# Performance work log

Measured on AMD Instinct MI355X. Metric: run time of the kernel, lower is better.

The kernel has to match this reference:

```python
import jax, jax.numpy as jnp
import numpy as np

MASK_ID = -100
L, D, HID, NH = 10, 768, 3072, 12
DH = D // NH
REACH = 2  # (sliding_window_size - 1) // 2 with window 5


def _layernorm(x, g, b, eps=1e-5):
    mu = x.mean(-1, keepdims=True)
    var = ((x - mu) ** 2).mean(-1, keepdims=True)
    return (x - mu) * jax.lax.rsqrt(var + eps) * g + b


def _adaln(x, temb, w, bb, g, be):
    # AdaLayerNormShiftScale: linear(silu(temb)) -> (scale, shift)
    e = jax.nn.silu(temb) @ w + bb
    scale, shift = jnp.split(e, 2, axis=-1)
    return _layernorm(x, g, be) * (1.0 + scale) + shift


def _timestep_emb(t):
    half = D // 2
    exponent = -np.log(10000.0) * jnp.arange(half, dtype=jnp.float32) / (half - 1.0)
    freq = jnp.exp(exponent)  # [half]
    emb = t.astype(jnp.float32)[..., None] * freq  # [b,s,half]
    return jnp.concatenate([jnp.sin(emb), jnp.cos(emb)], axis=-1)  # [b,s,D]


def setup_inputs():
    key = jax.random.key(0)
    ks = jax.random.split(key, 16)
    b, s = 4, 1024
    # packed token ids: 4 samples of 256 tokens (16x16 grid), last 64 tokens padding
    idx = np.arange(s)
    sid = idx // 256
    hpos = (idx % 256) // 16
    wpos = idx % 16
    sid = np.where(idx >= 960, MASK_ID, sid)
    tok = np.stack([sid, hpos, wpos], axis=-1)  # [s,3]
    token_ids = jnp.asarray(np.broadcast_to(tok, (b, s, 3)).copy(), dtype=jnp.int32)
    t = jax.random.randint(ks[0], (b, 1), 0, L + 1).astype(jnp.int32)
    t = jnp.broadcast_to(t, (b, s))

    def w(k, shape):
        return jax.random.normal(k, shape, jnp.float32) * 0.02

    return dict(
        x=jax.random.normal(ks[1], (b, s, D), jnp.float32),
        t=t,
        token_ids=token_ids,
        proj_in_w=w(ks[2], (D, D)), proj_in_b=jnp.zeros((D,), jnp.float32),
        h_emb=w(ks[3], (64, D)), w_emb=w(ks[4], (64, D)),
        adaln1_w=w(ks[5], (L, D, 2 * D)), adaln1_b=jnp.zeros((L, 2 * D), jnp.float32),
        ln1_g=jnp.ones((L, D), jnp.float32), ln1_b=jnp.zeros((L, D), jnp.float32),
        qkv_w=w(ks[6], (L, D, 3 * D)), qkv_b=jnp.zeros((L, 3 * D), jnp.float32),
        o_w=w(ks[7], (L, D, D)), o_b=jnp.zeros((L, D), jnp.float32),
        adaln2_w=w(ks[8], (L, D, 2 * D)), adaln2_b=jnp.zeros((L, 2 * D), jnp.float32),
        ln2_g=jnp.ones((L, D), jnp.float32), ln2_b=jnp.zeros((L, D), jnp.float32),
        fc1_w=w(ks[9], (L, D, HID)), fc1_b=jnp.zeros((L, HID), jnp.float32),
        fc2_w=w(ks[10], (L, HID, D)), fc2_b=jnp.zeros((L, D), jnp.float32),
        nout_w=w(ks[11], (D, 2 * D)), nout_b=jnp.zeros((2 * D,), jnp.float32),
        nout_g=jnp.ones((D,), jnp.float32), nout_beta=jnp.zeros((D,), jnp.float32),
    )


def _encoder(x, t, token_ids, proj_in_w, proj_in_b, h_emb, w_emb,
             adaln1_w, adaln1_b, ln1_g, ln1_b, qkv_w, qkv_b, o_w, o_b,
             adaln2_w, adaln2_b, ln2_g, ln2_b, fc1_w, fc1_b, fc2_w, fc2_b,
             nout_w, nout_b, nout_g, nout_beta):
    b, s, _ = x.shape
    sample_ids = token_ids[..., 0]          # [b,s]
    pos = token_ids[..., 1:]                # [b,s,2]
    x = x @ proj_in_w + proj_in_b
    x = x + h_emb[pos[..., 0]] + w_emb[pos[..., 1]]

    # block-sparse mask: same packed sample, Chebyshev sliding window, no padding queries
    same = sample_ids[:, :, None] == sample_ids[:, None, :]              # [b,s,s]
    cheby = jnp.abs(pos[:, :, None, :] - pos[:, None, :, :]).max(-1)      # [b,s,s]
    notpad_q = (sample_ids != MASK_ID)[:, :, None]
    mask = same & (cheby <= REACH) & notpad_q                             # [b,s,s]
    row_valid = mask.any(-1)[..., None]                                   # [b,s,1]

    temb = _timestep_emb(t)  # [b,s,D]
    scale = 1.0 / np.sqrt(DH)
    for i in range(L):
        h1 = _adaln(x, temb, adaln1_w[i], adaln1_b[i], ln1_g[i], ln1_b[i])
        qkv = h1 @ qkv_w[i] + qkv_b[i]
        q, k, v = jnp.split(qkv, 3, axis=-1)
        q = q.reshape(b, s, NH, DH)
        k = k.reshape(b, s, NH, DH)
        v = v.reshape(b, s, NH, DH)
        scores = jnp.einsum('bqhd,bkhd->bhqk', q, k) * scale
        scores = jnp.where(mask[:, None], scores, -1e30)
        attn = jax.nn.softmax(scores, axis=-1)
        o = jnp.einsum('bhqk,bkhd->bqhd', attn, v).reshape(b, s, D)
        o = jnp.where(row_valid, o, 0.0)  # fully-masked (padding) rows -> 0
        x = x + o @ o_w[i] + o_b[i]
        h2 = _adaln(x, temb, adaln2_w[i], adaln2_b[i], ln2_g[i], ln2_b[i])
        x = x + jax.nn.gelu(h2 @ fc1_w[i] + fc1_b[i], approximate=False) @ fc2_w[i] + fc2_b[i]
    x = _adaln(x, temb, nout_w, nout_b, nout_g, nout_beta)
    return x


def reference(x, t, token_ids, proj_in_w, proj_in_b, h_emb, w_emb,
              adaln1_w, adaln1_b, ln1_g, ln1_b, qkv_w, qkv_b, o_w, o_b,
              adaln2_w, adaln2_b, ln2_g, ln2_b, fc1_w, fc1_b, fc2_w, fc2_b,
              nout_w, nout_b, nout_g, nout_beta):
    return _encoder(x, t, token_ids, proj_in_w, proj_in_b, h_emb, w_emb,
                    adaln1_w, adaln1_b, ln1_g, ln1_b, qkv_w, qkv_b, o_w, o_b,
                    adaln2_w, adaln2_b, ln2_g, ln2_b, fc1_w, fc1_b, fc2_w, fc2_b,
                    nout_w, nout_b, nout_g, nout_beta)
```

## Files before the change

kernel.cpp:

```cpp
#include <hip/hip_runtime.h>
#include <hip/hip_bf16.h>
#include <math.h>

#define MASK_ID (-100)
#define SEQ 1024
#define BATCH 4
#define DMODEL 768
#define NHEAD 12
#define DHEAD 64
#define NLAYER 10
#define HIDDEN 3072

typedef unsigned short ushort_t;
typedef unsigned int uint_t;

__device__ __forceinline__ ushort_t f2bf(float f) {
    uint_t u = __float_as_uint(f);
    u = u + 0x7fffu + ((u >> 16) & 1u);
    return (ushort_t)(u >> 16);
}
__device__ __forceinline__ float bf2f(ushort_t u) {
    return __uint_as_float(((uint_t)u) << 16);
}

__device__ __forceinline__ void async_ld16(ushort_t* lds, const ushort_t* g) {
    __builtin_amdgcn_global_load_lds((__attribute__((address_space(1))) const void*)g,
                                     (__attribute__((address_space(3))) void*)lds, 16, 0, 0);
}

#define WAITVM(n) asm volatile("s_waitcnt vmcnt(" #n ")" ::: "memory")

__global__ void temb_silu_kernel(const int* __restrict__ t, float* __restrict__ stemb) {
    int b = blockIdx.x;
    int j = threadIdx.x;
    float tv = (float)t[b * SEQ];
    float freq = expf(-logf(10000.f) * (float)j / 383.f);
    float arg = tv * freq;
    float s = sinf(arg), c = cosf(arg);
    stemb[b * DMODEL + j]       = s / (1.f + expf(-s));
    stemb[b * DMODEL + 384 + j] = c / (1.f + expf(-c));
}

__global__ __launch_bounds__(256)
void adaln_partial_kernel(const float* __restrict__ stemb,
                          const float* __restrict__ a1w,
                          const float* __restrict__ a2w,
                          const float* __restrict__ nw,
                          float* __restrict__ partial) {
    int chunk = blockIdx.x;
    int kc    = blockIdx.y;
    int slot  = blockIdx.z;
    int tid = threadIdx.x;
    int col = chunk * 256 + tid;
    const float* W;
    if (slot == 20) W = nw;
    else {
        int i = slot >> 1;
        W = ((slot & 1) ? a2w : a1w) + (size_t)i * DMODEL * 2 * DMODEL;
    }
    __shared__ float sb[4 * 96];
    for (int idx = tid; idx < 4 * 96; idx += 256) {
        int bb = idx / 96, kk = idx % 96;
        sb[idx] = stemb[bb * DMODEL + kc * 96 + kk];
    }
    __syncthreads();
    const float* Wp = W + (size_t)(kc * 96) * (2 * DMODEL) + col;
    float a0 = 0.f, a1 = 0.f, a2 = 0.f, a3 = 0.f;
    #pragma unroll 4
    for (int kk = 0; kk < 96; ++kk) {
        float w = Wp[(size_t)kk * (2 * DMODEL)];
        a0 = fmaf(sb[kk], w, a0);
        a1 = fmaf(sb[96 + kk], w, a1);
        a2 = fmaf(sb[192 + kk], w, a2);
        a3 = fmaf(sb[288 + kk], w, a3);
    }
    size_t base = ((size_t)(slot * 8 + kc) * 4) * (2 * DMODEL) + col;
    partial[base + 0 * 2 * DMODEL] = a0;
    partial[base + 1 * 2 * DMODEL] = a1;
    partial[base + 2 * 2 * DMODEL] = a2;
    partial[base + 3 * 2 * DMODEL] = a3;
}

__global__ __launch_bounds__(256)
void adaln_reduce_kernel(const float* __restrict__ partial,
                         const float* __restrict__ a1b, const float* __restrict__ a2b,
                         const float* __restrict__ nb,
                         float* __restrict__ e_all) {
    int chunk = blockIdx.x;
    int slot  = blockIdx.y;
    int col = chunk * 256 + threadIdx.x;
    const float* bb;
    if (slot == 20) bb = nb;
    else {
        int i = slot >> 1;
        bb = ((slot & 1) ? a2b : a1b) + i * 2 * DMODEL;
    }
    float bias = bb[col];
    float s0 = bias, s1 = bias, s2 = bias, s3 = bias;
    #pragma unroll
    for (int kc = 0; kc < 8; ++kc) {
        size_t base = ((size_t)(slot * 8 + kc) * 4) * (2 * DMODEL) + col;
        s0 += partial[base + 0 * 2 * DMODEL];
        s1 += partial[base + 1 * 2 * DMODEL];
        s2 += partial[base + 2 * 2 * DMODEL];
        s3 += partial[base + 3 * 2 * DMODEL];
    }
    size_t o = (size_t)slot * 4 * (2 * DMODEL) + col;
    e_all[o + 0 * 2 * DMODEL] = s0;
    e_all[o + 1 * 2 * DMODEL] = s1;
    e_all[o + 2 * 2 * DMODEL] = s2;
    e_all[o + 3 * 2 * DMODEL] = s3;
}

__global__ __launch_bounds__(256)
void transpose_bf16_kernel(const float* __restrict__ in, ushort_t* __restrict__ out,
                           int R, int C) {
    __shared__ float tile[32][33];
    int tx = threadIdx.x & 31, ty = threadIdx.x >> 5;
    int c0 = blockIdx.x * 32, r0 = blockIdx.y * 32;
    #pragma unroll
    for (int i = 0; i < 4; ++i)
        tile[ty + 8 * i][tx] = in[(size_t)(r0 + ty + 8 * i) * C + c0 + tx];
    __syncthreads();
    #pragma unroll
    for (int i = 0; i < 4; ++i)
        out[(size_t)(c0 + ty + 8 * i) * R + r0 + tx] = f2bf(tile[tx][ty + 8 * i]);
}

__global__ __launch_bounds__(256)
void transpose_all_kernel(const float* __restrict__ w0, const float* __restrict__ w1,
                          const float* __restrict__ w2, const float* __restrict__ w3,
                          ushort_t* __restrict__ o0, ushort_t* __restrict__ o1,
                          ushort_t* __restrict__ o2, ushort_t* __restrict__ o3) {
    int layer = blockIdx.y;
    int id = blockIdx.x;
    const float* in; ushort_t* out; int R, C, tile_id, TX;
    if (id < 432) {
        in = w0 + (size_t)layer * DMODEL * 3 * DMODEL; out = o0 + (size_t)layer * 3 * DMODEL * DMODEL;
        R = DMODEL; C = 3 * DMODEL; tile_id = id; TX = 36;
    } else if (id < 576) {
        in = w1 + (size_t)layer * DMODEL * DMODEL; out = o1 + (size_t)layer * DMODEL * DMODEL;
        R = DMODEL; C = DMODEL; tile_id = id - 432; TX = 12;
    } else if (id < 1152) {
        in = w2 + (size_t)layer * DMODEL * HIDDEN; out = o2 + (size_t)layer * HIDDEN * DMODEL;
        R = DMODEL; C = HIDDEN; tile_id = id - 576; TX = 48;
    } else {
        in = w3 + (size_t)layer * HIDDEN * DMODEL; out = o3 + (size_t)layer * DMODEL * HIDDEN;
        R = HIDDEN; C = DMODEL; tile_id = id - 1152; TX = 12;
    }
    int c0 = (tile_id % TX) * 64, r0 = (tile_id / TX) * 64;
    __shared__ ushort_t tlb[64 * 65];
    int tid = threadIdx.x;
    #pragma unroll
    for (int i = 0; i < 16; ++i) {
        int idx = i * 256 + tid;
        int r = idx >> 6, c = idx & 63;
        tlb[r * 65 + c] = f2bf(in[(size_t)(r0 + r) * C + c0 + c]);
    }
    __syncthreads();
    #pragma unroll
    for (int j = 0; j < 8; ++j) {
        int idx = j * 256 + tid;
        int oc = idx >> 5, pr = idx & 31;
        uint_t pk = (uint_t)tlb[(pr * 2) * 65 + oc] | ((uint_t)tlb[(pr * 2 + 1) * 65 + oc] << 16);
        *(uint_t*)&out[(size_t)(c0 + oc) * R + r0 + pr * 2] = pk;
    }
}

__global__ __launch_bounds__(256)
void f32_to_bf16_kernel(const float* __restrict__ in, ushort_t* __restrict__ out, int n8) {
    int i = blockIdx.x * 256 + threadIdx.x;
    if (i >= n8) return;
    float4 a = ((const float4*)in)[2 * i];
    float4 b = ((const float4*)in)[2 * i + 1];
    uint4 o;
    o.x = (uint_t)f2bf(a.x) | ((uint_t)f2bf(a.y) << 16);
    o.y = (uint_t)f2bf(a.z) | ((uint_t)f2bf(a.w) << 16);
    o.z = (uint_t)f2bf(b.x) | ((uint_t)f2bf(b.y) << 16);
    o.w = (uint_t)f2bf(b.z) | ((uint_t)f2bf(b.w) << 16);
    ((uint4*)out)[i] = o;
}

template<int OUT_BF>
__global__ __launch_bounds__(256)
void ln_adaln_kernel(const float* __restrict__ in, void* __restrict__ outv,
                     const float* __restrict__ g, const float* __restrict__ be,
                     const float* __restrict__ e) {
    int wid = threadIdx.x >> 6, lane = threadIdx.x & 63;
    int row = blockIdx.x * 4 + wid;
    int b = row >> 10;
    const float* xr = in + (size_t)row * DMODEL;
    float v[12];
    float s = 0.f, ss = 0.f;
    #pragma unroll
    for (int j = 0; j < 12; ++j) {
        v[j] = xr[lane + j * 64];
        s += v[j];
        ss = fmaf(v[j], v[j], ss);
    }
    #pragma unroll
    for (int o = 1; o < 64; o <<= 1) { s += __shfl_xor(s, o); ss += __shfl_xor(ss, o); }
    float mu = s * (1.f / DMODEL);
    float var = ss * (1.f / DMODEL) - mu * mu;
    float rs = rsqrtf(var + 1e-5f);
    const float* esc = e + (size_t)b * (2 * DMODEL);
    #pragma unroll
    for (int j = 0; j < 12; ++j) {
        int c = lane + j * 64;
        float y = (v[j] - mu) * rs * g[c] + be[c];
        y = y * (1.f + esc[c]) + esc[DMODEL + c];
        if (OUT_BF) ((ushort_t*)outv)[(size_t)row * DMODEL + c] = f2bf(y);
        else        ((float*)outv)[(size_t)row * DMODEL + c] = y;
    }
}

__device__ __forceinline__ float gelu_exact(float x) {
    return 0.5f * x * (1.f + erff(x * 0.70710678118654752f));
}

template<int EPI>
__global__ __launch_bounds__(256, 3)
void gemm_bf16_big(const ushort_t* __restrict__ A, const ushort_t* __restrict__ Wt,
                   const float* __restrict__ bias, void* __restrict__ outv,
                   int M, int N, int K) {
    constexpr int BM = 128, BN = 128;
    using f32x4  = __attribute__((ext_vector_type(4))) float;
    using bf16x8 = __attribute__((ext_vector_type(8))) short;

    __shared__ __align__(16) ushort_t lds[(BM + BN) * 64];

    int tid = threadIdx.x;
    int lane = tid & 63, wid = tid >> 6;
    int wr = wid >> 1, wc = wid & 1;
    int l16 = lane & 15, lg = lane >> 4;
    int sw = l16 & 7;

    int nx = N / BN;
    int cpx = gridDim.x >> 3;
    int wg = blockIdx.x;
    int wgid = (wg & 7) * cpx + (wg >> 3);
    int bx = wgid % nx, by = wgid / nx;
    int bm0 = by * BM, bn0 = bx * BN;

    f32x4 acc[4][4];
    #pragma unroll
    for (int m = 0; m < 4; ++m)
        #pragma unroll
        for (int n = 0; n < 4; ++n)
            #pragma unroll
            for (int r = 0; r < 4; ++r) acc[m][n][r] = 0.f;

    const ushort_t* Abase = A + (size_t)bm0 * K;
    const ushort_t* Bbase = Wt + (size_t)bn0 * K;

    int nk = K >> 6;
    for (int kt = 0; kt < nk; ++kt) {
        #pragma unroll
        for (int s2 = 0; s2 < 4; ++s2) {
            int ca = s2 * 256 + tid;
            int rw = ca >> 3, kcs = (ca & 7) ^ (rw & 7);
            async_ld16(&lds[ca * 8], Abase + (size_t)rw * K + kt * 64 + kcs * 8);
        }
        #pragma unroll
        for (int s2 = 0; s2 < 4; ++s2) {
            int ca = s2 * 256 + tid;
            int rw = ca >> 3, kcs = (ca & 7) ^ (rw & 7);
            async_ld16(&lds[BM * 64 + ca * 8], Bbase + (size_t)rw * K + kt * 64 + kcs * 8);
        }
        WAITVM(0);
        __syncthreads();
        #pragma unroll
        for (int kk = 0; kk < 2; ++kk) {
            int csw = (kk * 4 + lg) ^ sw;
            bf16x8 af[4], bfr[4];
            #pragma unroll
            for (int m = 0; m < 4; ++m)
                af[m] = *(const bf16x8*)&lds[(wr * 64 + m * 16 + l16) * 64 + csw * 8];
            #pragma unroll
            for (int n = 0; n < 4; ++n)
                bfr[n] = *(const bf16x8*)&lds[BM * 64 + (wc * 64 + n * 16 + l16) * 64 + csw * 8];
            #pragma unroll
            for (int m = 0; m < 4; ++m)
                #pragma unroll
                for (int n = 0; n < 4; ++n)
                    acc[m][n] = __builtin_amdgcn_mfma_f32_16x16x32_bf16(af[m], bfr[n], acc[m][n], 0, 0, 0);
        }
        __syncthreads();
    }

    int r0 = bm0 + wr * 64, c0 = bn0 + wc * 64;
    #pragma unroll
    for (int m = 0; m < 4; ++m) {
        #pragma unroll
        for (int n = 0; n < 4; ++n) {
            int cc = c0 + n * 16 + l16;
            float bcol = bias[cc];
            #pragma unroll
            for (int r = 0; r < 4; ++r) {
                int row = r0 + m * 16 + lg * 4 + r;
                float v = acc[m][n][r] + bcol;
                if (EPI == 0) ((ushort_t*)outv)[(size_t)row * N + cc] = f2bf(v);
                else          ((ushort_t*)outv)[(size_t)row * N + cc] = f2bf(gelu_exact(v));
            }
        }
    }
}

template<int BM, int BN, int EPI, int OCC>
__global__ __launch_bounds__(256, OCC)
void gemm_bf16(const ushort_t* __restrict__ A, const ushort_t* __restrict__ Wt,
               const float* __restrict__ bias, void* __restrict__ outv,
               const float* __restrict__ emb_h, const float* __restrict__ emb_w,
               const int* __restrict__ tok,
               int M, int N, int K) {
    constexpr int WM = BM / 2, WN = BN / 2;
    constexpr int FM = WM / 16, FN = WN / 16;
    constexpr int BUF = (BM + BN) * 64;
    constexpr int LPT = (BM + BN) / 32;
    using f32x4  = __attribute__((ext_vector_type(4))) float;
    using bf16x8 = __attribute__((ext_vector_type(8))) short;

    __shared__ __align__(16) ushort_t lds[3 * BUF];

    int tid = threadIdx.x;
    int lane = tid & 63, wid = tid >> 6;
    int wr = wid >> 1, wc = wid & 1;
    int l16 = lane & 15, lg = lane >> 4;
    int sw = l16 & 7;

    int nx = N / BN;
    int cpx = gridDim.x >> 3;
    int wg = blockIdx.x;
    int wgid = (wg & 7) * cpx + (wg >> 3);
    int bx = wgid % nx, by = wgid / nx;
    int bm0 = by * BM, bn0 = bx * BN;

    f32x4 acc[FM][FN];
    #pragma unroll
    for (int m = 0; m < FM; ++m)
        #pragma unroll
        for (int n = 0; n < FN; ++n)
            #pragma unroll
            for (int r = 0; r < 4; ++r) acc[m][n][r] = 0.f;

    const ushort_t* Abase = A + (size_t)bm0 * K;
    const ushort_t* Bbase = Wt + (size_t)bn0 * K;

    #define STAGE(bufi, kt)                                                             \
        do {                                                                            \
            _Pragma("unroll")                                                           \
            for (int s2 = 0; s2 < BM / 32; ++s2) {                                      \
                int ca = s2 * 256 + tid;                                                \
                int rw = ca >> 3, kcs = (ca & 7) ^ (rw & 7);                            \
                async_ld16(&lds[(bufi) * BUF + ca * 8],                                 \
                           Abase + (size_t)rw * K + (kt) * 64 + kcs * 8);               \
            }                                                                           \
            _Pragma("unroll")                                                           \
            for (int s2 = 0; s2 < BN / 32; ++s2) {                                      \
                int ca = s2 * 256 + tid;                                                \
                int rw = ca >> 3, kcs = (ca & 7) ^ (rw & 7);                            \
                async_ld16(&lds[(bufi) * BUF + BM * 64 + ca * 8],                       \
                           Bbase + (size_t)rw * K + (kt) * 64 + kcs * 8);               \
            }                                                                           \
        } while (0)

    int nk = K >> 6;
    STAGE(0, 0);
    STAGE(1, 1);
    int bufi = 0;
    for (int kt = 0; kt < nk; ++kt) {
        int nxt = bufi + 2; if (nxt >= 3) nxt -= 3;
        if (kt + 2 < nk) {
            STAGE(nxt, kt + 2);
            if constexpr (LPT == 4) WAITVM(8); else WAITVM(12);
        } else if (kt + 1 < nk) {
            if constexpr (LPT == 4) WAITVM(4); else WAITVM(6);
        } else {
            WAITVM(0);
        }
        __builtin_amdgcn_s_barrier();
        __builtin_amdgcn_s_setprio(1);
        #pragma unroll
        for (int kk = 0; kk < 2; ++kk) {
            bf16x8 af[FM], bfr[FN];
            #pragma unroll
            for (int m = 0; m < FM; ++m) {
                int row = wr * WM + m * 16 + l16;
                int csw = (kk * 4 + lg) ^ sw;
                af[m] = *(const bf16x8*)&lds[bufi * BUF + row * 64 + csw * 8];
            }
            #pragma unroll
            for (int n = 0; n < FN; ++n) {
                int row = wc * WN + n * 16 + l16;
                int csw = (kk * 4 + lg) ^ sw;
                bfr[n] = *(const bf16x8*)&lds[bufi * BUF + BM * 64 + row * 64 + csw * 8];
            }
            #pragma unroll
            for (int m = 0; m < FM; ++m)
                #pragma unroll
                for (int n = 0; n < FN; ++n)
                    acc[m][n] = __builtin_amdgcn_mfma_f32_16x16x32_bf16(af[m], bfr[n], acc[m][n], 0, 0, 0);
        }
        __builtin_amdgcn_s_setprio(0);
        __builtin_amdgcn_s_barrier();
        ++bufi; if (bufi >= 3) bufi = 0;
    }
    #undef STAGE

    int r0 = bm0 + wr * WM, c0 = bn0 + wc * WN;
    #pragma unroll
    for (int m = 0; m < FM; ++m) {
        #pragma unroll
        for (int n = 0; n < FN; ++n) {
            int cc = c0 + n * 16 + l16;
            float bcol = bias[cc];
            #pragma unroll
            for (int r = 0; r < 4; ++r) {
                int row = r0 + m * 16 + lg * 4 + r;
                float v = acc[m][n][r] + bcol;
                if (EPI == 0) {
                    ((ushort_t*)outv)[(size_t)row * N + cc] = f2bf(v);
                } else if (EPI == 1) {
                    int p0 = tok[row * 3 + 1], p1 = tok[row * 3 + 2];
                    v += emb_h[p0 * DMODEL + cc] + emb_w[p1 * DMODEL + cc];
                    ((float*)outv)[(size_t)row * N + cc] = v;
                } else if (EPI == 2) {
                    float* op = (float*)outv + (size_t)row * N + cc;
                    *op = *op + v;
                } else {
                    ((ushort_t*)outv)[(size_t)row * N + cc] = f2bf(gelu_exact(v));
                }
            }
        }
    }
}

__global__ __launch_bounds__(256)
void attn_kernel(const ushort_t* __restrict__ qkv, const int* __restrict__ tok,
                 ushort_t* __restrict__ o_out) {
    int tid = threadIdx.x;
    int u = tid >> 2, part = tid & 3;
    int q = blockIdx.x * 16 + (u & 15);
    int h = blockIdx.y * 4 + (u >> 4);
    int b = blockIdx.z;
    int m = b * SEQ + q;
    ushort_t* op = o_out + (size_t)m * DMODEL + h * DHEAD + part * 16;
    int sid = tok[m * 3];
    if (sid == MASK_ID) {
        uint4 z = {0u, 0u, 0u, 0u};
        ((uint4*)op)[0] = z;
        ((uint4*)op)[1] = z;
        return;
    }
    int qh = tok[m * 3 + 1], qw = tok[m * 3 + 2];
    const ushort_t* qp = qkv + (size_t)m * (3 * DMODEL) + h * DHEAD + part * 16;
    float qv[16], ov[16];
    {
        uint4 u0 = ((const uint4*)qp)[0];
        uint4 u1 = ((const uint4*)qp)[1];
        qv[0] = bf2f(u0.x & 0xffff); qv[1] = bf2f(u0.x >> 16);
        qv[2] = bf2f(u0.y & 0xffff); qv[3] = bf2f(u0.y >> 16);
        qv[4] = bf2f(u0.z & 0xffff); qv[5] = bf2f(u0.z >> 16);
        qv[6] = bf2f(u0.w & 0xffff); qv[7] = bf2f(u0.w >> 16);
        qv[8]  = bf2f(u1.x & 0xffff); qv[9]  = bf2f(u1.x >> 16);
        qv[10] = bf2f(u1.y & 0xffff); qv[11] = bf2f(u1.y >> 16);
        qv[12] = bf2f(u1.z & 0xffff); qv[13] = bf2f(u1.z >> 16);
        qv[14] = bf2f(u1.w & 0xffff); qv[15] = bf2f(u1.w >> 16);
    }
    #pragma unroll
    for (int i = 0; i < 16; ++i) ov[i] = 0.f;
    float mx = -1e30f, den = 0.f;
    for (int dh = -2; dh <= 2; ++dh) {
        for (int dw = -2; dw <= 2; ++dw) {
            int kq = q + dh * 16 + dw;
            if (kq < 0 || kq >= SEQ) continue;
            int km = b * SEQ + kq;
            if (tok[km * 3] != sid) continue;
            int kh2 = tok[km * 3 + 1], kw2 = tok[km * 3 + 2];
            int adh = kh2 - qh; if (adh < 0) adh = -adh;
            int adw = kw2 - qw; if (adw < 0) adw = -adw;
            if (adh > 2 || adw > 2) continue;
            const ushort_t* kp = qkv + (size_t)km * (3 * DMODEL) + DMODEL + h * DHEAD + part * 16;
            float dot;
            {
                uint4 u0 = ((const uint4*)kp)[0];
                uint4 u1 = ((const uint4*)kp)[1];
                dot = qv[0] * bf2f(u0.x & 0xffff);
                dot = fmaf(qv[1], bf2f(u0.x >> 16), dot);
                dot = fmaf(qv[2], bf2f(u0.y & 0xffff), dot);
                dot = fmaf(qv[3], bf2f(u0.y >> 16), dot);
                dot = fmaf(qv[4], bf2f(u0.z & 0xffff), dot);
                dot = fmaf(qv[5], bf2f(u0.z >> 16), dot);
                dot = fmaf(qv[6], bf2f(u0.w & 0xffff), dot);
                dot = fmaf(qv[7], bf2f(u0.w >> 16), dot);
                dot = fmaf(qv[8],  bf2f(u1.x & 0xffff), dot);
                dot = fmaf(qv[9],  bf2f(u1.x >> 16), dot);
                dot = fmaf(qv[10], bf2f(u1.y & 0xffff), dot);
                dot = fmaf(qv[11], bf2f(u1.y >> 16), dot);
                dot = fmaf(qv[12], bf2f(u1.z & 0xffff), dot);
                dot = fmaf(qv[13], bf2f(u1.z >> 16), dot);
                dot = fmaf(qv[14], bf2f(u1.w & 0xffff), dot);
                dot = fmaf(qv[15], bf2f(u1.w >> 16), dot);
            }
            dot += __shfl_xor(dot, 1);
            dot += __shfl_xor(dot, 2);
            float sc = dot * 0.125f;
            float nm = fmaxf(mx, sc);
            float c1 = expf(mx - nm);
            float c2 = expf(sc - nm);
            den = den * c1 + c2;
            const ushort_t* vp = qkv + (size_t)km * (3 * DMODEL) + 2 * DMODEL + h * DHEAD + part * 16;
            {
                uint4 u0 = ((const uint4*)vp)[0];
                uint4 u1 = ((const uint4*)vp)[1];
                ov[0] = ov[0] * c1 + c2 * bf2f(u0.x & 0xffff);
                ov[1] = ov[1] * c1 + c2 * bf2f(u0.x >> 16);
                ov[2] = ov[2] * c1 + c2 * bf2f(u0.y & 0xffff);
                ov[3] = ov[3] * c1 + c2 * bf2f(u0.y >> 16);
                ov[4] = ov[4] * c1 + c2 * bf2f(u0.z & 0xffff);
                ov[5] = ov[5] * c1 + c2 * bf2f(u0.z >> 16);
                ov[6] = ov[6] * c1 + c2 * bf2f(u0.w & 0xffff);
                ov[7] = ov[7] * c1 + c2 * bf2f(u0.w >> 16);
                ov[8]  = ov[8]  * c1 + c2 * bf2f(u1.x & 0xffff);
                ov[9]  = ov[9]  * c1 + c2 * bf2f(u1.x >> 16);
                ov[10] = ov[10] * c1 + c2 * bf2f(u1.y & 0xffff);
                ov[11] = ov[11] * c1 + c2 * bf2f(u1.y >> 16);
                ov[12] = ov[12] * c1 + c2 * bf2f(u1.z & 0xffff);
                ov[13] = ov[13] * c1 + c2 * bf2f(u1.z >> 16);
                ov[14] = ov[14] * c1 + c2 * bf2f(u1.w & 0xffff);
                ov[15] = ov[15] * c1 + c2 * bf2f(u1.w >> 16);
            }
            mx = nm;
        }
    }
    float inv = 1.f / den;
    uint4 o0, o1;
    o0.x = (uint_t)f2bf(ov[0] * inv) | ((uint_t)f2bf(ov[1] * inv) << 16);
    o0.y = (uint_t)f2bf(ov[2] * inv) | ((uint_t)f2bf(ov[3] * inv) << 16);
    o0.z = (uint_t)f2bf(ov[4] * inv) | ((uint_t)f2bf(ov[5] * inv) << 16);
    o0.w = (uint_t)f2bf(ov[6] * inv) | ((uint_t)f2bf(ov[7] * inv) << 16);
    o1.x = (uint_t)f2bf(ov[8]  * inv) | ((uint_t)f2bf(ov[9]  * inv) << 16);
    o1.y = (uint_t)f2bf(ov[10] * inv) | ((uint_t)f2bf(ov[11] * inv) << 16);
    o1.z = (uint_t)f2bf(ov[12] * inv) | ((uint_t)f2bf(ov[13] * inv) << 16);
    o1.w = (uint_t)f2bf(ov[14] * inv) | ((uint_t)f2bf(ov[15] * inv) << 16);
    ((uint4*)op)[0] = o0;
    ((uint4*)op)[1] = o1;
}

extern "C" void kernel_launch(void* const* d_in, const int* in_sizes, int n_in,
                              void* d_out, int out_size, void* d_ws, size_t ws_size,
                              hipStream_t stream) {
    const float* x_in      = (const float*)d_in[0];
    const int*   t         = (const int*)d_in[1];
    const int*   tok       = (const int*)d_in[2];
    const float* proj_in_w = (const float*)d_in[3];
    const float* proj_in_b = (const float*)d_in[4];
    const float* h_emb     = (const float*)d_in[5];
    const float* w_emb     = (const float*)d_in[6];
    const float* adaln1_w  = (const float*)d_in[7];
    const float* adaln1_b  = (const float*)d_in[8];
    const float* ln1_g     = (const float*)d_in[9];
    const float* ln1_b     = (const float*)d_in[10];
    const float* qkv_w     = (const float*)d_in[11];
    const float* qkv_b     = (const float*)d_in[12];
    const float* o_w       = (const float*)d_in[13];
    const float* o_b       = (const float*)d_in[14];
    const float* adaln2_w  = (const float*)d_in[15];
    const float* adaln2_b  = (const float*)d_in[16];
    const float* ln2_g     = (const float*)d_in[17];
    const float* ln2_b     = (const float*)d_in[18];
    const float* fc1_w     = (const float*)d_in[19];
    const float* fc1_b     = (const float*)d_in[20];
    const float* fc2_w     = (const float*)d_in[21];
    const float* fc2_b     = (const float*)d_in[22];
    const float* nout_w    = (const float*)d_in[23];
    const float* nout_b    = (const float*)d_in[24];
    const float* nout_g    = (const float*)d_in[25];
    const float* nout_beta = (const float*)d_in[26];

    const int M = BATCH * SEQ;

    float* stemb   = (float*)d_ws;
    float* e_all   = stemb + BATCH * DMODEL;
    float* partial = e_all + 21 * BATCH * 2 * DMODEL;
    ushort_t* h_bf   = (ushort_t*)(partial + 21 * 8 * 4 * 2 * DMODEL);
    ushort_t* qkv_bf = h_bf + (size_t)M * DMODEL;
    ushort_t* hid_bf = qkv_bf + (size_t)M * 3 * DMODEL;
    ushort_t* projT  = hid_bf + (size_t)M * HIDDEN;
    ushort_t* qkvT_a = projT + (size_t)DMODEL * DMODEL;
    ushort_t* oT_a   = qkvT_a + (size_t)NLAYER * 3 * DMODEL * DMODEL;
    ushort_t* fc1T_a = oT_a + (size_t)NLAYER * DMODEL * DMODEL;
    ushort_t* fc2T_a = fc1T_a + (size_t)NLAYER * DMODEL * HIDDEN;
    float* x = (float*)d_out;

    temb_silu_kernel<<<BATCH, 384, 0, stream>>>(t, stemb);
    adaln_partial_kernel<<<dim3(6, 8, 2 * NLAYER + 1), 256, 0, stream>>>(
        stemb, adaln1_w, adaln2_w, nout_w, partial);
    adaln_reduce_kernel<<<dim3(6, 2 * NLAYER + 1), 256, 0, stream>>>(
        partial, adaln1_b, adaln2_b, nout_b, e_all);

    transpose_all_kernel<<<dim3(1728, NLAYER), 256, 0, stream>>>(
        qkv_w, o_w, fc1_w, fc2_w, qkvT_a, oT_a, fc1T_a, fc2T_a);
    transpose_bf16_kernel<<<dim3(DMODEL / 32, DMODEL / 32), 256, 0, stream>>>(proj_in_w, projT, DMODEL, DMODEL);

    f32_to_bf16_kernel<<<(M * DMODEL / 8 + 255) / 256, 256, 0, stream>>>(x_in, h_bf, M * DMODEL / 8);
    gemm_bf16<64, 64, 1, 3><<<(DMODEL / 64) * (M / 64), 256, 0, stream>>>(
        h_bf, projT, proj_in_b, x, h_emb, w_emb, tok, M, DMODEL, DMODEL);

    for (int i = 0; i < NLAYER; ++i) {
        ln_adaln_kernel<1><<<M / 4, 256, 0, stream>>>(
            x, h_bf, ln1_g + i * DMODEL, ln1_b + i * DMODEL,
            e_all + (size_t)(2 * i) * BATCH * 2 * DMODEL);
        gemm_bf16_big<0><<<(3 * DMODEL / 128) * (M / 128), 256, 0, stream>>>(
            h_bf, qkvT_a + (size_t)i * 3 * DMODEL * DMODEL, qkv_b + i * 3 * DMODEL,
            qkv_bf, M, 3 * DMODEL, DMODEL);
        attn_kernel<<<dim3(SEQ / 16, NHEAD / 4, BATCH), 256, 0, stream>>>(qkv_bf, tok, h_bf);
        gemm_bf16<64, 64, 2, 3><<<(DMODEL / 64) * (M / 64), 256, 0, stream>>>(
            h_bf, oT_a + (size_t)i * DMODEL * DMODEL, o_b + i * DMODEL,
            x, nullptr, nullptr, nullptr, M, DMODEL, DMODEL);
        ln_adaln_kernel<1><<<M / 4, 256, 0, stream>>>(
            x, h_bf, ln2_g + i * DMODEL, ln2_b + i * DMODEL,
            e_all + (size_t)(2 * i + 1) * BATCH * 2 * DMODEL);
        gemm_bf16_big<3><<<(HIDDEN / 128) * (M / 128), 256, 0, stream>>>(
            h_bf, fc1T_a + (size_t)i * DMODEL * HIDDEN, fc1_b + i * HIDDEN,
            hid_bf, M, HIDDEN, DMODEL);
        gemm_bf16<64, 64, 2, 3><<<(DMODEL / 64) * (M / 64), 256, 0, stream>>>(
            hid_bf, fc2T_a + (size_t)i * DMODEL * HIDDEN, fc2_b + i * DMODEL,
            x, nullptr, nullptr, nullptr, M, DMODEL, HIDDEN);
    }

    ln_adaln_kernel<0><<<M / 4, 256, 0, stream>>>(
        x, x, nout_g, nout_beta, e_all + (size_t)(2 * NLAYER) * BATCH * 2 * DMODEL);
}
```

Baseline: 1.685 ms.

## Merge weight-prep kernels into one launch and retile the fc2 GEMM

```diff
diff --git a/kernel.cpp b/kernel.cpp
--- a/kernel.cpp
+++ b/kernel.cpp
@@ -41,44 +41,114 @@
     stemb[b * DMODEL + 384 + j] = c / (1.f + expf(-c));
 }
 
+#define PREP_GRID 20400
 __global__ __launch_bounds__(256)
-void adaln_partial_kernel(const float* __restrict__ stemb,
-                          const float* __restrict__ a1w,
-                          const float* __restrict__ a2w,
-                          const float* __restrict__ nw,
-                          float* __restrict__ partial) {
-    int chunk = blockIdx.x;
-    int kc    = blockIdx.y;
-    int slot  = blockIdx.z;
+void prep_all_kernel(const float* __restrict__ w0, const float* __restrict__ w1,
+                     const float* __restrict__ w2, const float* __restrict__ w3,
+                     ushort_t* __restrict__ o0, ushort_t* __restrict__ o1,
+                     ushort_t* __restrict__ o2, ushort_t* __restrict__ o3,
+                     const float* __restrict__ proj_in_w, ushort_t* __restrict__ projT,
+                     const float* __restrict__ x_in, ushort_t* __restrict__ h_bf,
+                     const float* __restrict__ stemb,
+                     const float* __restrict__ a1w, const float* __restrict__ a2w,
+                     const float* __restrict__ nw, float* __restrict__ partial) {
+    __shared__ __align__(16) char smem[64 * 65 * 2];
+    int gid = blockIdx.x;
     int tid = threadIdx.x;
-    int col = chunk * 256 + tid;
-    const float* W;
-    if (slot == 20) W = nw;
-    else {
-        int i = slot >> 1;
-        W = ((slot & 1) ? a2w : a1w) + (size_t)i * DMODEL * 2 * DMODEL;
-    }
-    __shared__ float sb[4 * 96];
-    for (int idx = tid; idx < 4 * 96; idx += 256) {
-        int bb = idx / 96, kk = idx % 96;
-        sb[idx] = stemb[bb * DMODEL + kc * 96 + kk];
-    }
-    __syncthreads();
-    const float* Wp = W + (size_t)(kc * 96) * (2 * DMODEL) + col;
-    float a0 = 0.f, a1 = 0.f, a2 = 0.f, a3 = 0.f;
-    #pragma unroll 4
-    for (int kk = 0; kk < 96; ++kk) {
-        float w = Wp[(size_t)kk * (2 * DMODEL)];
-        a0 = fmaf(sb[kk], w, a0);
-        a1 = fmaf(sb[96 + kk], w, a1);
-        a2 = fmaf(sb[192 + kk], w, a2);
-        a3 = fmaf(sb[288 + kk], w, a3);
-    }
-    size_t base = ((size_t)(slot * 8 + kc) * 4) * (2 * DMODEL) + col;
-    partial[base + 0 * 2 * DMODEL] = a0;
-    partial[base + 1 * 2 * DMODEL] = a1;
-    partial[base + 2 * 2 * DMODEL] = a2;
-    partial[base + 3 * 2 * DMODEL] = a3;
+
+    if (gid < 17280) {
+        int layer = gid / 1728;
+        int id = gid % 1728;
+        const float* in; ushort_t* out; int R, C, tile_id, TX;
+        if (id < 432) {
+            in = w0 + (size_t)layer * DMODEL * 3 * DMODEL; out = o0 + (size_t)layer * 3 * DMODEL * DMODEL;
+            R = DMODEL; C = 3 * DMODEL; tile_id = id; TX = 36;
+        } else if (id < 576) {
+            in = w1 + (size_t)layer * DMODEL * DMODEL; out = o1 + (size_t)layer * DMODEL * DMODEL;
+            R = DMODEL; C = DMODEL; tile_id = id - 432; TX = 12;
+        } else if (id < 1152) {
+            in = w2 + (size_t)layer * DMODEL * HIDDEN; out = o2 + (size_t)layer * HIDDEN * DMODEL;
+            R = DMODEL; C = HIDDEN; tile_id = id - 576; TX = 48;
+        } else {
+            in = w3 + (size_t)layer * HIDDEN * DMODEL; out = o3 + (size_t)layer * DMODEL * HIDDEN;
+            R = HIDDEN; C = DMODEL; tile_id = id - 1152; TX = 12;
+        }
+        int c0 = (tile_id % TX) * 64, r0 = (tile_id / TX) * 64;
+        ushort_t* tlb = (ushort_t*)smem;
+        #pragma unroll
+        for (int i = 0; i < 4; ++i) {
+            int idx = i * 256 + tid;
+            int r = idx >> 4, c4 = (idx & 15) * 4;
+            float4 v = *(const float4*)&in[(size_t)(r0 + r) * C + c0 + c4];
+            tlb[r * 65 + c4 + 0] = f2bf(v.x);
+            tlb[r * 65 + c4 + 1] = f2bf(v.y);
+            tlb[r * 65 + c4 + 2] = f2bf(v.z);
+            tlb[r * 65 + c4 + 3] = f2bf(v.w);
+        }
+        __syncthreads();
+        #pragma unroll
+        for (int j = 0; j < 8; ++j) {
+            int idx = j * 256 + tid;
+            int oc = idx >> 5, pr = idx & 31;
+            uint_t pk = (uint_t)tlb[(pr * 2) * 65 + oc] | ((uint_t)tlb[(pr * 2 + 1) * 65 + oc] << 16);
+            *(uint_t*)&out[(size_t)(c0 + oc) * R + r0 + pr * 2] = pk;
+        }
+    } else if (gid < 17856) {
+        int s = gid - 17280;
+        int c0 = (s % 24) * 32, r0 = (s / 24) * 32;
+        float* tile = (float*)smem;
+        int tx = tid & 31, ty = tid >> 5;
+        #pragma unroll
+        for (int i = 0; i < 4; ++i)
+            tile[(ty + 8 * i) * 33 + tx] = proj_in_w[(size_t)(r0 + ty + 8 * i) * DMODEL + c0 + tx];
+        __syncthreads();
+        #pragma unroll
+        for (int i = 0; i < 4; ++i)
+            projT[(size_t)(c0 + ty + 8 * i) * DMODEL + r0 + tx] = f2bf(tile[tx * 33 + ty + 8 * i]);
+    } else if (gid < 19392) {
+        int i = (gid - 17856) * 256 + tid;
+        float4 a = ((const float4*)x_in)[2 * i];
+        float4 b = ((const float4*)x_in)[2 * i + 1];
+        uint4 o;
+        o.x = (uint_t)f2bf(a.x) | ((uint_t)f2bf(a.y) << 16);
+        o.y = (uint_t)f2bf(a.z) | ((uint_t)f2bf(a.w) << 16);
+        o.z = (uint_t)f2bf(b.x) | ((uint_t)f2bf(b.y) << 16);
+        o.w = (uint_t)f2bf(b.z) | ((uint_t)f2bf(b.w) << 16);
+        ((uint4*)h_bf)[i] = o;
+    } else {
+        int s3 = gid - 19392;
+        int chunk = s3 % 6;
+        int kc = (s3 / 6) % 8;
+        int slot = s3 / 48;
+        int col = chunk * 256 + tid;
+        const float* W;
+        if (slot == 20) W = nw;
+        else {
+            int i = slot >> 1;
+            W = ((slot & 1) ? a2w : a1w) + (size_t)i * DMODEL * 2 * DMODEL;
+        }
+        float* sb = (float*)smem;
+        for (int idx = tid; idx < 4 * 96; idx += 256) {
+            int bb = idx / 96, kk = idx % 96;
+            sb[idx] = stemb[bb * DMODEL + kc * 96 + kk];
+        }
+        __syncthreads();
+        const float* Wp = W + (size_t)(kc * 96) * (2 * DMODEL) + col;
+        float a0 = 0.f, a1 = 0.f, a2 = 0.f, a3 = 0.f;
+        #pragma unroll 4
+        for (int kk = 0; kk < 96; ++kk) {
+            float w = Wp[(size_t)kk * (2 * DMODEL)];
+            a0 = fmaf(sb[kk], w, a0);
+            a1 = fmaf(sb[96 + kk], w, a1);
+            a2 = fmaf(sb[192 + kk], w, a2);
+            a3 = fmaf(sb[288 + kk], w, a3);
+        }
+        size_t base = ((size_t)(slot * 8 + kc) * 4) * (2 * DMODEL) + col;
+        partial[base + 0 * 2 * DMODEL] = a0;
+        partial[base + 1 * 2 * DMODEL] = a1;
+        partial[base + 2 * 2 * DMODEL] = a2;
+        partial[base + 3 * 2 * DMODEL] = a3;
+    }
 }
 
 __global__ __launch_bounds__(256)
@@ -110,75 +180,6 @@
     e_all[o + 1 * 2 * DMODEL] = s1;
     e_all[o + 2 * 2 * DMODEL] = s2;
     e_all[o + 3 * 2 * DMODEL] = s3;
-}
-
-__global__ __launch_bounds__(256)
-void transpose_bf16_kernel(const float* __restrict__ in, ushort_t* __restrict__ out,
-                           int R, int C) {
-    __shared__ float tile[32][33];
-    int tx = threadIdx.x & 31, ty = threadIdx.x >> 5;
-    int c0 = blockIdx.x * 32, r0 = blockIdx.y * 32;
-    #pragma unroll
-    for (int i = 0; i < 4; ++i)
-        tile[ty + 8 * i][tx] = in[(size_t)(r0 + ty + 8 * i) * C + c0 + tx];
-    __syncthreads();
-    #pragma unroll
-    for (int i = 0; i < 4; ++i)
-        out[(size_t)(c0 + ty + 8 * i) * R + r0 + tx] = f2bf(tile[tx][ty + 8 * i]);
-}
-
-__global__ __launch_bounds__(256)
-void transpose_all_kernel(const float* __restrict__ w0, const float* __restrict__ w1,
-                          const float* __restrict__ w2, const float* __restrict__ w3,
-                          ushort_t* __restrict__ o0, ushort_t* __restrict__ o1,
-                          ushort_t* __restrict__ o2, ushort_t* __restrict__ o3) {
-    int layer = blockIdx.y;
-    int id = blockIdx.x;
-    const float* in; ushort_t* out; int R, C, tile_id, TX;
-    if (id < 432) {
-        in = w0 + (size_t)layer * DMODEL * 3 * DMODEL; out = o0 + (size_t)layer * 3 * DMODEL * DMODEL;
-        R = DMODEL; C = 3 * DMODEL; tile_id = id; TX = 36;
-    } else if (id < 576) {
-        in = w1 + (size_t)layer * DMODEL * DMODEL; out = o1 + (size_t)layer * DMODEL * DMODEL;
-        R = DMODEL; C = DMODEL; tile_id = id - 432; TX = 12;
-    } else if (id < 1152) {
-        in = w2 + (size_t)layer * DMODEL * HIDDEN; out = o2 + (size_t)layer * HIDDEN * DMODEL;
-        R = DMODEL; C = HIDDEN; tile_id = id - 576; TX = 48;
-    } else {
-        in = w3 + (size_t)layer * HIDDEN * DMODEL; out = o3 + (size_t)layer * DMODEL * HIDDEN;
-        R = HIDDEN; C = DMODEL; tile_id = id - 1152; TX = 12;
-    }
-    int c0 = (tile_id % TX) * 64, r0 = (tile_id / TX) * 64;
-    __shared__ ushort_t tlb[64 * 65];
-    int tid = threadIdx.x;
-    #pragma unroll
-    for (int i = 0; i < 16; ++i) {
-        int idx = i * 256 + tid;
-        int r = idx >> 6, c = idx & 63;
-        tlb[r * 65 + c] = f2bf(in[(size_t)(r0 + r) * C + c0 + c]);
-    }
-    __syncthreads();
-    #pragma unroll
-    for (int j = 0; j < 8; ++j) {
-        int idx = j * 256 + tid;
-        int oc = idx >> 5, pr = idx & 31;
-        uint_t pk = (uint_t)tlb[(pr * 2) * 65 + oc] | ((uint_t)tlb[(pr * 2 + 1) * 65 + oc] << 16);
-        *(uint_t*)&out[(size_t)(c0 + oc) * R + r0 + pr * 2] = pk;
-    }
-}
-
-__global__ __launch_bounds__(256)
-void f32_to_bf16_kernel(const float* __restrict__ in, ushort_t* __restrict__ out, int n8) {
-    int i = blockIdx.x * 256 + threadIdx.x;
-    if (i >= n8) return;
-    float4 a = ((const float4*)in)[2 * i];
-    float4 b = ((const float4*)in)[2 * i + 1];
-    uint4 o;
-    o.x = (uint_t)f2bf(a.x) | ((uint_t)f2bf(a.y) << 16);
-    o.y = (uint_t)f2bf(a.z) | ((uint_t)f2bf(a.w) << 16);
-    o.z = (uint_t)f2bf(b.x) | ((uint_t)f2bf(b.y) << 16);
-    o.w = (uint_t)f2bf(b.z) | ((uint_t)f2bf(b.w) << 16);
-    ((uint4*)out)[i] = o;
 }
 
 template<int OUT_BF>
@@ -594,16 +595,12 @@
     float* x = (float*)d_out;
 
     temb_silu_kernel<<<BATCH, 384, 0, stream>>>(t, stemb);
-    adaln_partial_kernel<<<dim3(6, 8, 2 * NLAYER + 1), 256, 0, stream>>>(
-        stemb, adaln1_w, adaln2_w, nout_w, partial);
+    prep_all_kernel<<<PREP_GRID, 256, 0, stream>>>(
+        qkv_w, o_w, fc1_w, fc2_w, qkvT_a, oT_a, fc1T_a, fc2T_a,
+        proj_in_w, projT, x_in, h_bf, stemb, adaln1_w, adaln2_w, nout_w, partial);
     adaln_reduce_kernel<<<dim3(6, 2 * NLAYER + 1), 256, 0, stream>>>(
         partial, adaln1_b, adaln2_b, nout_b, e_all);
 
-    transpose_all_kernel<<<dim3(1728, NLAYER), 256, 0, stream>>>(
-        qkv_w, o_w, fc1_w, fc2_w, qkvT_a, oT_a, fc1T_a, fc2T_a);
-    transpose_bf16_kernel<<<dim3(DMODEL / 32, DMODEL / 32), 256, 0, stream>>>(proj_in_w, projT, DMODEL, DMODEL);
-
-    f32_to_bf16_kernel<<<(M * DMODEL / 8 + 255) / 256, 256, 0, stream>>>(x_in, h_bf, M * DMODEL / 8);
     gemm_bf16<64, 64, 1, 3><<<(DMODEL / 64) * (M / 64), 256, 0, stream>>>(
         h_bf, projT, proj_in_b, x, h_emb, w_emb, tok, M, DMODEL, DMODEL);
 
@@ -624,7 +621,7 @@
         gemm_bf16_big<3><<<(HIDDEN / 128) * (M / 128), 256, 0, stream>>>(
             h_bf, fc1T_a + (size_t)i * DMODEL * HIDDEN, fc1_b + i * HIDDEN,
             hid_bf, M, HIDDEN, DMODEL);
-        gemm_bf16<64, 64, 2, 3><<<(DMODEL / 64) * (M / 64), 256, 0, stream>>>(
+        gemm_bf16<128, 64, 2, 2><<<(DMODEL / 64) * (M / 128), 256, 0, stream>>>(
             hid_bf, fc2T_a + (size_t)i * DMODEL * HIDDEN, fc2_b + i * DMODEL,
             x, nullptr, nullptr, nullptr, M, DMODEL, HIDDEN);
     }
```

Measured after the change: 1.663 ms. About the same (-1.3%).
